# Kernel tuning notes

Measured on AMD Instinct MI355X. Metric: run time of the kernel, lower is better.

The kernel has to match this reference:

```python
import jax, jax.numpy as jnp
import numpy as np

DMODEL = 1024

def setup_inputs() -> dict:
    key = jax.random.key(0)
    ks = jax.random.split(key, 7)
    scale = 1.0 / np.sqrt(DMODEL)
    x = jax.random.normal(ks[0], (4, 2048, DMODEL), dtype=jnp.float32)
    Wq = jax.random.normal(ks[1], (DMODEL, DMODEL), dtype=jnp.float32) * scale
    bq = jnp.zeros((DMODEL,), dtype=jnp.float32)
    Wk = jax.random.normal(ks[2], (DMODEL, DMODEL), dtype=jnp.float32) * scale
    bk = jnp.zeros((DMODEL,), dtype=jnp.float32)
    Wv = jax.random.normal(ks[3], (DMODEL, DMODEL), dtype=jnp.float32) * scale
    bv = jnp.zeros((DMODEL,), dtype=jnp.float32)
    return {"x": x, "Wq": Wq, "bq": bq, "Wk": Wk, "bk": bk, "Wv": Wv, "bv": bv}

def reference(x, Wq, bq, Wk, bk, Wv, bv):
    # QKV projections: [b, s, d]
    q = jnp.einsum('bsd,de->bse', x, Wq) + bq
    k = jnp.einsum('bsd,de->bse', x, Wk) + bk
    v = jnp.einsum('bsd,de->bse', x, Wv) + bv
    # scaled dot-product attention, full [b, s, s] score matrix (as in source)
    scores = jnp.einsum('bqd,bkd->bqk', q, k) / jnp.sqrt(jnp.asarray(q.shape[-1], q.dtype))
    weights = jax.nn.softmax(scores, axis=-1)
    return jnp.einsum('bqk,bkd->bqd', weights, v)
```

## Files before the change

### kernel.cpp

```cpp
#include <hip/hip_runtime.h>

typedef unsigned short u16;
typedef __attribute__((ext_vector_type(8))) short short8;
typedef __attribute__((ext_vector_type(4))) short short4v;
typedef __attribute__((ext_vector_type(4))) float f32x4;


__device__ __forceinline__ u16 f2bf(float f) {
  union { float f; unsigned u; } c; c.f = f;
  unsigned u = c.u;
  unsigned r = u + 0x7fffu + ((u >> 16) & 1u);
  return (u16)(r >> 16);
}

__device__ __forceinline__ float bf2f(u16 b) {
  union { unsigned u; float f; } c; c.u = ((unsigned)b) << 16;
  return c.f;
}

__device__ __forceinline__ void load_lds16(const void* g, void* l) {
  __builtin_amdgcn_global_load_lds(
      (__attribute__((address_space(1))) void*)(__UINTPTR_TYPE__)(g),
      (__attribute__((address_space(3))) void*)(l),
      16, 0, 0);
}

template <int N> __device__ __forceinline__ void vm_wait() {
  if constexpr (N == 0) asm volatile("s_waitcnt vmcnt(0)");
  else if constexpr (N == 3) asm volatile("s_waitcnt vmcnt(3)");
  else if constexpr (N == 4) asm volatile("s_waitcnt vmcnt(4)");
}

template <int BM, int MODE>
__global__ __launch_bounds__(512)
void gemm256(const u16* __restrict__ A, const u16* __restrict__ Bt,
             void* __restrict__ C0, void* __restrict__ C1,
             const float* __restrict__ b0, const float* __restrict__ b1,
             const float* __restrict__ b2,
             int K, int lda, int ldb, int ldc, float scale,
             long zsA, long zsB, long zsC)
{
  constexpr int MREP = BM / 32;
  constexpr int LA   = BM / 128;
  constexpr int BOFF = BM * 64;
  constexpr int LDSE = BM * 64 + 16384;
  __shared__ __align__(16) u16 lds[2][LDSE];

  A  += (long)blockIdx.z * zsA;
  Bt += (long)blockIdx.z * zsB;

  int bxi, byi;
  if (MODE == 0 || MODE == 3) {
    const int gw   = gridDim.x;
    const int nwg  = gw * gridDim.y;
    const int orig = blockIdx.x + gw * blockIdx.y;
    const int s    = (orig & 7) * (nwg >> 3) + (orig >> 3);
    bxi = s % gw; byi = s / gw;
  } else {
    bxi = blockIdx.x; byi = blockIdx.y;
  }

  const int t    = threadIdx.x;
  const int lane = t & 63;
  const int wave = t >> 6;
  const int wr   = wave >> 2;
  const int wc   = wave & 3;
  const long brow = (long)byi * BM;
  const long bcol = (long)bxi * 256;

  f32x4 acc[MREP][4];
#pragma unroll
  for (int m = 0; m < MREP; ++m)
#pragma unroll
    for (int n = 0; n < 4; ++n)
#pragma unroll
      for (int j = 0; j < 4; ++j) acc[m][n][j] = 0.f;

  const int frA  = wr * (BM / 2) + (lane & 15);
  const int kAsw = (((lane >> 4) ^ ((frA >> 1) & 3)) * 8);
  const int frB  = wc * 64 + (lane & 15);
  const int kBsw = (((lane >> 4) ^ ((frB >> 1) & 3)) * 8);

  const int sr  = t >> 2;
  const int ssl = ((t & 3) ^ ((sr >> 1) & 3)) * 8;
  const u16* gA = A  + (size_t)(brow + sr) * lda + ssl;
  const u16* gB = Bt + (size_t)(bcol + sr) * ldb + ssl;
  const int NT = K >> 6;

#define STAGE_A(nb, kt1, ks) do {                                   \
    u16* d = &lds[(nb)][(ks) * (BM * 32) + t * 8];                  \
    const u16* g = gA + (size_t)(kt1) * 64 + (ks) * 32;             \
    load_lds16(g, d);                                               \
    if (LA == 2) load_lds16(g + (size_t)128 * lda, d + 4096);       \
  } while (0)

#define STAGE_B(nb, kt1, ks) do {                                   \
    u16* d = &lds[(nb)][BOFF + (ks) * 8192 + t * 8];                \
    const u16* g = gB + (size_t)(kt1) * 64 + (ks) * 32;             \
    load_lds16(g, d);                                               \
    load_lds16(g + (size_t)128 * ldb, d + 4096);                    \
  } while (0)

#define PHASE2(ks, STG, VM) {                                                    \
    _Pragma("unroll")                                                            \
    for (int i = 0; i < MREP; ++i)                                               \
      af[i] = *(const short8*)&bufA[(ks) * (BM * 32) +                           \
                 (size_t)(frA + i * 16) * 32 + kAsw];                            \
    _Pragma("unroll")                                                            \
    for (int n = 0; n < 4; ++n)                                                  \
      bf[n] = *(const short8*)&bufB[(ks) * 8192 +                                \
                 (size_t)(frB + n * 16) * 32 + kBsw];                            \
    STG;                                                                         \
    __builtin_amdgcn_s_barrier();                                                \
    asm volatile("s_waitcnt lgkmcnt(0)");                                        \
    __builtin_amdgcn_s_setprio(1);                                               \
    _Pragma("unroll")                                                            \
    for (int i = 0; i < MREP; ++i)                                               \
      _Pragma("unroll")                                                          \
      for (int n = 0; n < 4; ++n)                                                \
        acc[i][n] = __builtin_amdgcn_mfma_f32_16x16x32_bf16(                     \
            af[i], bf[n], acc[i][n], 0, 0, 0);                                   \
    __builtin_amdgcn_s_setprio(0);                                               \
    VM;                                                                          \
    __builtin_amdgcn_s_barrier();                                                \
  }

  STAGE_A(0, 0, 0); STAGE_B(0, 0, 0); STAGE_A(0, 0, 1); STAGE_B(0, 0, 1);
  vm_wait<0>();
  __builtin_amdgcn_s_barrier();

  short8 af[MREP], bf[4];
  for (int kt = 0; kt < NT - 1; ++kt) {
    const u16* bufA = &lds[kt & 1][0];
    const u16* bufB = bufA + BOFF;
    const int nb = (kt + 1) & 1;
    PHASE2(0, { STAGE_A(nb, kt + 1, 0); STAGE_B(nb, kt + 1, 0); }, vm_wait<LA + 2>())
    PHASE2(1, { STAGE_A(nb, kt + 1, 1); STAGE_B(nb, kt + 1, 1); }, vm_wait<LA + 2>())
  }
  {
    const u16* bufA = &lds[(NT - 1) & 1][0];
    const u16* bufB = bufA + BOFF;
    PHASE2(0, (void)0, vm_wait<0>())
    PHASE2(1, (void)0, (void)0)
  }
#undef PHASE2
#undef STAGE_A
#undef STAGE_B

  const int dcol = lane & 15;
  const int dr4  = (lane >> 4) * 4;
  if (MODE == 0) {
    const int which = (int)(bcol >> 10);
    const float sc = which ? 1.0f : scale;
    const float* bb = which ? b1 : b0;
    u16* dst = (u16*)C0 + (long)which * (8192L * 1024);
#pragma unroll
    for (int m = 0; m < MREP; ++m) {
#pragma unroll
      for (int n = 0; n < 4; ++n) {
        const long cp   = (bcol - ((long)which << 10)) + wc * 64 + n * 16 + dcol;
        const long row0 = brow + wr * (BM / 2) + m * 16 + dr4;
        const float bias = bb[cp];
#pragma unroll
        for (int j = 0; j < 4; ++j)
          dst[(row0 + j) * 1024 + cp] = f2bf((acc[m][n][j] + bias) * sc);
      }
    }
  } else if (MODE == 3) {
    constexpr int SMSK = BM / 4 - 1;
    u16* sm = (u16*)lds;
#pragma unroll
    for (int m = 0; m < MREP; ++m) {
#pragma unroll
      for (int n = 0; n < 4; ++n) {
        const int cpl = wc * 64 + n * 16 + dcol;
        const int r0l = wr * (BM / 2) + m * 16 + dr4;
        const float bias = b2[bcol + cpl];
        short4v w;
#pragma unroll
        for (int j = 0; j < 4; ++j) w[j] = (short)f2bf(acc[m][n][j] + bias);
        *(short4v*)&sm[cpl * BM + (((r0l >> 2) ^ (cpl & SMSK)) << 2)] = w;
      }
    }
    __syncthreads();
    u16* dst = (u16*)C1;
#pragma unroll
    for (int it = 0; it < BM / 16; ++it) {
      const int idx = it * 512 + t;
      const int i  = idx / (BM / 8);
      const int ch = idx & (BM / 8 - 1);
      const short4v lo = *(const short4v*)&sm[i * BM + ((((ch * 2)    ) ^ (i & SMSK)) << 2)];
      const short4v hi = *(const short4v*)&sm[i * BM + ((((ch * 2) + 1) ^ (i & SMSK)) << 2)];
      short8 o;
      o[0] = lo[0]; o[1] = lo[1]; o[2] = lo[2]; o[3] = lo[3];
      o[4] = hi[0]; o[5] = hi[1]; o[6] = hi[2]; o[7] = hi[3];
      *(short8*)&dst[(bcol + i) * 8192 + brow + ch * 8] = o;
    }
  } else if (MODE == 5) {
    float* rs = (float*)C1 + (long)blockIdx.z * 2048;
    u16* dst = (u16*)C0 + (long)blockIdx.z * zsC;
#pragma unroll
    for (int m = 0; m < MREP; ++m) {
      const long row0 = brow + wr * (BM / 2) + m * 16 + dr4;
      float rv[4] = {0.f, 0.f, 0.f, 0.f};
#pragma unroll
      for (int n = 0; n < 4; ++n) {
        const long col = bcol + wc * 64 + n * 16 + dcol;
#pragma unroll
        for (int j = 0; j < 4; ++j) {
          const float p = __expf(acc[m][n][j]);
          dst[(row0 + j) * ldc + col] = f2bf(p);
          rv[j] += p;
        }
      }
#pragma unroll
      for (int j = 0; j < 4; ++j) {
#pragma unroll
        for (int o = 1; o < 16; o <<= 1) rv[j] += __shfl_xor(rv[j], o);
      }
      if (dcol == 0) {
#pragma unroll
        for (int j = 0; j < 4; ++j) atomicAdd(&rs[row0 + j], rv[j]);
      }
    }
  } else if (MODE == 6) {
    const float* rs = (const float*)C1 + (long)blockIdx.z * 2048;
#pragma unroll
    for (int m = 0; m < MREP; ++m) {
      const long row0 = brow + wr * (BM / 2) + m * 16 + dr4;
      float inv[4];
#pragma unroll
      for (int j = 0; j < 4; ++j) inv[j] = 1.0f / rs[row0 + j];
#pragma unroll
      for (int n = 0; n < 4; ++n) {
        const long col = bcol + wc * 64 + n * 16 + dcol;
#pragma unroll
        for (int j = 0; j < 4; ++j)
          ((float*)C0)[(long)blockIdx.z * zsC + (row0 + j) * ldc + col] =
              acc[m][n][j] * inv[j];
      }
    }
  } else {
#pragma unroll
    for (int m = 0; m < MREP; ++m) {
#pragma unroll
      for (int n = 0; n < 4; ++n) {
        const long col  = bcol + wc * 64 + n * 16 + dcol;
        const long row0 = brow + wr * (BM / 2) + m * 16 + dr4;
        if (MODE == 1) {
#pragma unroll
          for (int j = 0; j < 4; ++j)
            ((u16*)C0)[(long)blockIdx.z * zsC + (row0 + j) * ldc + col] =
                f2bf(acc[m][n][j] * scale);
        } else {
#pragma unroll
          for (int j = 0; j < 4; ++j)
            ((float*)C0)[(long)blockIdx.z * zsC + (row0 + j) * ldc + col] =
                acc[m][n][j];
        }
      }
    }
  }
}

__global__ __launch_bounds__(256)
void cvt_bf16(const float* __restrict__ in, u16* __restrict__ out, int n4)
{
  int i = blockIdx.x * 256 + threadIdx.x;
  const int stride = gridDim.x * 256;
  for (; i < n4; i += stride) {
    const float4 f = ((const float4*)in)[i];
    ushort4 u;
    u.x = f2bf(f.x); u.y = f2bf(f.y); u.z = f2bf(f.z); u.w = f2bf(f.w);
    ((ushort4*)out)[i] = u;
  }
}

__global__ __launch_bounds__(256)
void wtrans(const float* __restrict__ W, u16* __restrict__ Wt)
{
  __shared__ u16 tile[32][33];
  const int tx = threadIdx.x;
  const int ty = threadIdx.y;
  const int bx = blockIdx.x * 32;
  const int by = blockIdx.y * 32;
#pragma unroll
  for (int i = 0; i < 4; ++i)
    tile[ty + i * 8][tx] = f2bf(W[(size_t)(by + ty + i * 8) * 1024 + bx + tx]);
  __syncthreads();
#pragma unroll
  for (int i = 0; i < 4; ++i)
    Wt[(size_t)(bx + ty + i * 8) * 1024 + by + tx] = tile[tx][ty + i * 8];
}

extern "C" void kernel_launch(void* const* d_in, const int* in_sizes, int n_in,
                              void* d_out, int out_size, void* d_ws, size_t ws_size,
                              hipStream_t stream)
{
  const float* x  = (const float*)d_in[0];
  const float* Wq = (const float*)d_in[1];
  const float* bq = (const float*)d_in[2];
  const float* Wk = (const float*)d_in[3];
  const float* bk = (const float*)d_in[4];
  const float* Wv = (const float*)d_in[5];
  const float* bv = (const float*)d_in[6];
  float* out = (float*)d_out;
  char* ws = (char*)d_ws;

  const size_t MB = (size_t)1 << 20;
  const float qscale = 0.03125f;
  const long  SO = 2048L * 1024;

  u16* Qb   = (u16*)(ws);
  u16* Kb   = (u16*)(ws + 16 * MB);
  u16* Vt   = (u16*)(ws + 32 * MB);
  u16* Sc   = (u16*)(ws + 48 * MB);
  u16* xb   = (u16*)(ws + 48 * MB);
  u16* Wcat = (u16*)(ws + 80 * MB);
  float* rowsum = (float*)(ws + 80 * MB);

  cvt_bf16<<<2048, 256, 0, stream>>>(x, xb, (4 * 2048 * 1024) / 4);
  dim3 tb(32, 8), tg(32, 32);
  wtrans<<<tg, tb, 0, stream>>>(Wq, Wcat);
  wtrans<<<tg, tb, 0, stream>>>(Wk, Wcat + 1024 * 1024);
  wtrans<<<tg, tb, 0, stream>>>(Wv, Wcat + 2 * 1024 * 1024);

  gemm256<256, 0><<<dim3(8, 32), 512, 0, stream>>>(
      xb, Wcat, Qb, nullptr, bq, bk, nullptr,
      1024, 1024, 1024, 1024, qscale, 0, 0, 0);

  gemm256<128, 3><<<dim3(4, 64), 512, 0, stream>>>(
      xb, Wcat + 2 * 1024 * 1024, nullptr, Vt, nullptr, nullptr, bv,
      1024, 1024, 1024, 1024, 1.0f, 0, 0, 0);

  hipMemsetAsync(rowsum, 0, 4 * 2048 * sizeof(float), stream);

  gemm256<256, 5><<<dim3(8, 8, 4), 512, 0, stream>>>(
      Qb, Kb, Sc, rowsum, nullptr, nullptr, nullptr,
      1024, 1024, 1024, 2048, 1.0f, SO, SO, 2048L * 2048);

  gemm256<128, 6><<<dim3(4, 16, 4), 512, 0, stream>>>(
      Sc, Vt, out, rowsum, nullptr, nullptr, nullptr,
      2048, 2048, 8192, 1024, 1.0f, 2048L * 2048, 2048, SO);
}
```

Before: 168.7 us.

## Fold Q and K projections into a precomputed Wq·Wkᵀ product

Rewrites the scores as x·(Wq·Wkᵀ)·xᵀ plus rank-one bias terms. A small 1024³ GEMM builds M = Wq·Wkᵀ, one GEMM forms T = x·M, and the score GEMM then multiplies T against bf16 x directly. This replaces the separate Q and K projections and cuts total matmul work. The bias cross-terms come from new helper kernels: bias_w computes the Wq·bk and Wk·bq vectors plus the constant bq·bk, and uv_vec forms the per-row bias terms. Row-sum atomics and the memset are also replaced by per-wave partial sums that the PV kernel reduces in shared memory. The cost is extra small launches, and a possible precision change because M is rounded to bf16.

```diff
diff --git a/kernel.cpp b/kernel.cpp
--- a/kernel.cpp
+++ b/kernel.cpp
@@ -50,7 +50,7 @@
   Bt += (long)blockIdx.z * zsB;
 
   int bxi, byi;
-  if (MODE == 0 || MODE == 3) {
+  if (MODE == 3) {
     const int gw   = gridDim.x;
     const int nwg  = gw * gridDim.y;
     const int orig = blockIdx.x + gw * blockIdx.y;
@@ -149,24 +149,7 @@
 
   const int dcol = lane & 15;
   const int dr4  = (lane >> 4) * 4;
-  if (MODE == 0) {
-    const int which = (int)(bcol >> 10);
-    const float sc = which ? 1.0f : scale;
-    const float* bb = which ? b1 : b0;
-    u16* dst = (u16*)C0 + (long)which * (8192L * 1024);
-#pragma unroll
-    for (int m = 0; m < MREP; ++m) {
-#pragma unroll
-      for (int n = 0; n < 4; ++n) {
-        const long cp   = (bcol - ((long)which << 10)) + wc * 64 + n * 16 + dcol;
-        const long row0 = brow + wr * (BM / 2) + m * 16 + dr4;
-        const float bias = bb[cp];
-#pragma unroll
-        for (int j = 0; j < 4; ++j)
-          dst[(row0 + j) * 1024 + cp] = f2bf((acc[m][n][j] + bias) * sc);
-      }
-    }
-  } else if (MODE == 3) {
+  if (MODE == 3) {
     constexpr int SMSK = BM / 4 - 1;
     u16* sm = (u16*)lds;
 #pragma unroll
@@ -175,10 +158,11 @@
       for (int n = 0; n < 4; ++n) {
         const int cpl = wc * 64 + n * 16 + dcol;
         const int r0l = wr * (BM / 2) + m * 16 + dr4;
-        const float bias = b2[bcol + cpl];
+        const float bias = b2 ? b2[bcol + cpl] : 0.f;
         short4v w;
 #pragma unroll
-        for (int j = 0; j < 4; ++j) w[j] = (short)f2bf(acc[m][n][j] + bias);
+        for (int j = 0; j < 4; ++j)
+          w[j] = (short)f2bf((acc[m][n][j] + bias) * scale);
         *(short4v*)&sm[cpl * BM + (((r0l >> 2) ^ (cpl & SMSK)) << 2)] = w;
       }
     }
@@ -194,21 +178,28 @@
       short8 o;
       o[0] = lo[0]; o[1] = lo[1]; o[2] = lo[2]; o[3] = lo[3];
       o[4] = hi[0]; o[5] = hi[1]; o[6] = hi[2]; o[7] = hi[3];
-      *(short8*)&dst[(bcol + i) * 8192 + brow + ch * 8] = o;
+      *(short8*)&dst[(size_t)(bcol + i) * ldc + brow + ch * 8] = o;
     }
   } else if (MODE == 5) {
-    float* rs = (float*)C1 + (long)blockIdx.z * 2048;
+    const float* ug = b0 + (long)blockIdx.z * 2048;
+    const float* vg = b1 + (long)blockIdx.z * 2048;
+    const float c0v = b2[0];
+    float* part = (float*)C1 + ((long)blockIdx.z * 32 + (bxi * 4 + wc)) * 2048;
     u16* dst = (u16*)C0 + (long)blockIdx.z * zsC;
 #pragma unroll
     for (int m = 0; m < MREP; ++m) {
       const long row0 = brow + wr * (BM / 2) + m * 16 + dr4;
+      float uval[4];
+#pragma unroll
+      for (int j = 0; j < 4; ++j) uval[j] = ug[row0 + j] + c0v;
       float rv[4] = {0.f, 0.f, 0.f, 0.f};
 #pragma unroll
       for (int n = 0; n < 4; ++n) {
         const long col = bcol + wc * 64 + n * 16 + dcol;
+        const float vv = vg[col];
 #pragma unroll
         for (int j = 0; j < 4; ++j) {
-          const float p = __expf(acc[m][n][j]);
+          const float p = __expf(acc[m][n][j] + uval[j] + vv);
           dst[(row0 + j) * ldc + col] = f2bf(p);
           rv[j] += p;
         }
@@ -220,17 +211,30 @@
       }
       if (dcol == 0) {
 #pragma unroll
-        for (int j = 0; j < 4; ++j) atomicAdd(&rs[row0 + j], rv[j]);
+        for (int j = 0; j < 4; ++j) part[row0 + j] = rv[j];
       }
     }
   } else if (MODE == 6) {
-    const float* rs = (const float*)C1 + (long)blockIdx.z * 2048;
+    const float* part = (const float*)C1 + (long)blockIdx.z * 32 * 2048;
+    float* smf = (float*)lds;
+    {
+      const int r = t >> 2, q4 = t & 3;
+      float s = 0.f;
+#pragma unroll
+      for (int i = 0; i < 8; ++i) s += part[(q4 * 8 + i) * 2048 + brow + r];
+      smf[r * 4 + q4] = s;
+    }
+    __syncthreads();
+    if (t < 128)
+      smf[512 + t] = 1.0f / (smf[4 * t] + smf[4 * t + 1] + smf[4 * t + 2] + smf[4 * t + 3]);
+    __syncthreads();
 #pragma unroll
     for (int m = 0; m < MREP; ++m) {
       const long row0 = brow + wr * (BM / 2) + m * 16 + dr4;
+      const int  rl   = (int)(row0 - brow);
       float inv[4];
 #pragma unroll
-      for (int j = 0; j < 4; ++j) inv[j] = 1.0f / rs[row0 + j];
+      for (int j = 0; j < 4; ++j) inv[j] = smf[512 + rl + j];
 #pragma unroll
       for (int n = 0; n < 4; ++n) {
         const long col = bcol + wc * 64 + n * 16 + dcol;
@@ -291,6 +295,66 @@
 #pragma unroll
   for (int i = 0; i < 4; ++i)
     Wt[(size_t)(bx + ty + i * 8) * 1024 + by + tx] = tile[tx][ty + i * 8];
+}
+
+__global__ __launch_bounds__(256)
+void bias_w(const float* __restrict__ Wq, const float* __restrict__ Wk,
+            const float* __restrict__ bq, const float* __restrict__ bk,
+            float* __restrict__ w1, float* __restrict__ w2,
+            float* __restrict__ c0, float qs)
+{
+  const int wave = threadIdx.x >> 6, lane = threadIdx.x & 63;
+  const int row = blockIdx.x * 4 + wave;
+  const float* mat = (row < 1024) ? (Wq + (size_t)row * 1024)
+                                  : (Wk + (size_t)(row - 1024) * 1024);
+  const float* bv = (row < 1024) ? bk : bq;
+  float s = 0.f;
+#pragma unroll
+  for (int i = 0; i < 4; ++i) {
+    const float4 mv = *(const float4*)&mat[lane * 4 + i * 256];
+    const float4 bb = *(const float4*)&bv[lane * 4 + i * 256];
+    s += mv.x * bb.x + mv.y * bb.y + mv.z * bb.z + mv.w * bb.w;
+  }
+#pragma unroll
+  for (int o = 32; o; o >>= 1) s += __shfl_xor(s, o);
+  if (lane == 0) ((row < 1024) ? w1 : w2)[row & 1023] = s * qs;
+  if (blockIdx.x == 0 && wave == 0) {
+    float c = 0.f;
+#pragma unroll
+    for (int i = 0; i < 4; ++i) {
+      const float4 a = *(const float4*)&bq[lane * 4 + i * 256];
+      const float4 b = *(const float4*)&bk[lane * 4 + i * 256];
+      c += a.x * b.x + a.y * b.y + a.z * b.z + a.w * b.w;
+    }
+#pragma unroll
+    for (int o = 32; o; o >>= 1) c += __shfl_xor(c, o);
+    if (lane == 0) c0[0] = c * qs;
+  }
+}
+
+__global__ __launch_bounds__(256)
+void uv_vec(const u16* __restrict__ xb, const float* __restrict__ w1,
+            const float* __restrict__ w2, float* __restrict__ u,
+            float* __restrict__ v)
+{
+  const int wave = threadIdx.x >> 6, lane = threadIdx.x & 63;
+  const long row = (long)blockIdx.x * 4 + wave;
+  const u16* xr = xb + row * 1024;
+  float su = 0.f, sv = 0.f;
+#pragma unroll
+  for (int h = 0; h < 2; ++h) {
+    const int d0 = lane * 8 + h * 512;
+    const short8 xv = *(const short8*)&xr[d0];
+#pragma unroll
+    for (int k = 0; k < 8; ++k) {
+      const float xf = bf2f((u16)xv[k]);
+      su += xf * w1[d0 + k];
+      sv += xf * w2[d0 + k];
+    }
+  }
+#pragma unroll
+  for (int o = 32; o; o >>= 1) { su += __shfl_xor(su, o); sv += __shfl_xor(sv, o); }
+  if (lane == 0) { u[row] = su; v[row] = sv; }
 }
 
 extern "C" void kernel_launch(void* const* d_in, const int* in_sizes, int n_in,
@@ -311,35 +375,48 @@
   const float qscale = 0.03125f;
   const long  SO = 2048L * 1024;
 
-  u16* Qb   = (u16*)(ws);
-  u16* Kb   = (u16*)(ws + 16 * MB);
+  u16* T    = (u16*)(ws);
+  u16* xb   = (u16*)(ws + 16 * MB);
   u16* Vt   = (u16*)(ws + 32 * MB);
   u16* Sc   = (u16*)(ws + 48 * MB);
-  u16* xb   = (u16*)(ws + 48 * MB);
-  u16* Wcat = (u16*)(ws + 80 * MB);
-  float* rowsum = (float*)(ws + 80 * MB);
+  u16* Wqb  = (u16*)(ws + 80 * MB);
+  u16* Wkb  = (u16*)(ws + 82 * MB);
+  u16* Wvt  = (u16*)(ws + 84 * MB);
+  u16* Mt   = (u16*)(ws + 86 * MB);
+  float* partial = (float*)(ws + 88 * MB);
+  float* uvec    = (float*)(ws + 89 * MB);
+  float* vvec    = (float*)(ws + 89 * MB + 32768);
+  float* c0p     = (float*)(ws + 89 * MB + 65536);
 
   cvt_bf16<<<2048, 256, 0, stream>>>(x, xb, (4 * 2048 * 1024) / 4);
-  dim3 tb(32, 8), tg(32, 32);
-  wtrans<<<tg, tb, 0, stream>>>(Wq, Wcat);
-  wtrans<<<tg, tb, 0, stream>>>(Wk, Wcat + 1024 * 1024);
-  wtrans<<<tg, tb, 0, stream>>>(Wv, Wcat + 2 * 1024 * 1024);
-
-  gemm256<256, 0><<<dim3(8, 32), 512, 0, stream>>>(
-      xb, Wcat, Qb, nullptr, bq, bk, nullptr,
+  cvt_bf16<<<512, 256, 0, stream>>>(Wq, Wqb, (1024 * 1024) / 4);
+  cvt_bf16<<<512, 256, 0, stream>>>(Wk, Wkb, (1024 * 1024) / 4);
+  {
+    dim3 tb(32, 8), tg(32, 32);
+    wtrans<<<tg, tb, 0, stream>>>(Wv, Wvt);
+  }
+  bias_w<<<512, 256, 0, stream>>>(Wq, Wk, bq, bk, uvec, vvec, c0p, qscale);
+
+  gemm256<128, 3><<<dim3(4, 8), 512, 0, stream>>>(
+      Wqb, Wkb, nullptr, Mt, nullptr, nullptr, nullptr,
       1024, 1024, 1024, 1024, qscale, 0, 0, 0);
 
   gemm256<128, 3><<<dim3(4, 64), 512, 0, stream>>>(
-      xb, Wcat + 2 * 1024 * 1024, nullptr, Vt, nullptr, nullptr, bv,
+      xb, Wvt, nullptr, Vt, nullptr, nullptr, bv,
+      1024, 1024, 1024, 8192, 1.0f, 0, 0, 0);
+
+  bias_w<<<512, 256, 0, stream>>>(Wq, Wk, bq, bk, partial, partial + 1024, c0p, qscale);
+  uv_vec<<<2048, 256, 0, stream>>>(xb, partial, partial + 1024, uvec, vvec);
+
+  gemm256<256, 1><<<dim3(4, 32), 512, 0, stream>>>(
+      xb, Mt, T, nullptr, nullptr, nullptr, nullptr,
       1024, 1024, 1024, 1024, 1.0f, 0, 0, 0);
 
-  hipMemsetAsync(rowsum, 0, 4 * 2048 * sizeof(float), stream);
-
   gemm256<256, 5><<<dim3(8, 8, 4), 512, 0, stream>>>(
-      Qb, Kb, Sc, rowsum, nullptr, nullptr, nullptr,
+      T, xb, Sc, partial, uvec, vvec, c0p,
       1024, 1024, 1024, 2048, 1.0f, SO, SO, 2048L * 2048);
 
   gemm256<128, 6><<<dim3(4, 16, 4), 512, 0, stream>>>(
-      Sc, Vt, out, rowsum, nullptr, nullptr, nullptr,
+      Sc, Vt, out, partial, nullptr, nullptr, nullptr,
       2048, 2048, 8192, 1024, 1.0f, 2048L * 2048, 2048, SO);
 }
```

Result: slower. 190.4 us (+12.8%).
